# Optimization experiments

Hardware: AMD Instinct MI355X
Metric: run time of the kernel (lower is better)

Reference implementation:

```python
import jax, jax.numpy as jnp
import numpy as np

B, L, C = 16, 450, 768
MID = 256
K = 8912
TEMP = 0.07
ENT_TEMP = 0.01
EPS_NORM = 1e-12


def _l2norm(v):
    n = jnp.sqrt(jnp.sum(v * v, axis=-1, keepdims=True))
    return v / jnp.maximum(n, EPS_NORM)


def setup_inputs() -> dict:
    key = jax.random.key(0)
    k1, k2, k3, k4 = jax.random.split(key, 4)
    x = jax.random.normal(k1, (B, L, C), dtype=jnp.float32)
    W_down = jax.random.normal(k2, (C, MID), dtype=jnp.float32) * (1.0 / np.sqrt(C))
    b_down = jnp.zeros((MID,), dtype=jnp.float32)
    bound = 1.0 / np.sqrt(MID)
    embedding = jax.random.uniform(k3, (K, MID), dtype=jnp.float32, minval=-bound, maxval=bound)
    return {"x": x, "W_down": W_down, "b_down": b_down, "embedding": embedding}


def reference(x, W_down, b_down, embedding):
    Bx, Lx, Cx = x.shape
    # down projection: [B,L,C] -> [B,L,MID]
    z = jnp.einsum('blc,cm->blm', x, W_down) + b_down
    zf = z.reshape(Bx * Lx, MID)
    zn = _l2norm(zf)                       # [N, MID]
    en = _l2norm(embedding)                # [K, MID]
    # squared euclidean distance on the unit sphere: ||a-b||^2 = 2 - 2 a.b
    d = 2.0 - 2.0 * jnp.einsum('nm,km->nk', zn, en)   # [N, K]
    idx = jnp.argmin(d, axis=1)            # [N]
    # codebook usage (no-grad stats)
    occ = jnp.bincount(idx, length=K)
    code_book_usage = jnp.mean((occ > 0).astype(jnp.float32))
    # soft assignment probs (hard_quant branch)
    logits = -d / TEMP
    probs = jax.nn.softmax(logits, axis=1)
    z_q = en[idx]                          # [N, MID]
    vq_loss = jnp.mean((z_q - jax.lax.stop_gradient(zn)) ** 2)
    commit_loss = jnp.mean((jax.lax.stop_gradient(z_q) - zn) ** 2)
    # straight-through estimator
    z_q_ste = zn + jax.lax.stop_gradient(z_q - zn)
    # entropy loss on affinity = -d at entropy temperature
    fa = -d / ENT_TEMP
    p = jax.nn.softmax(fa, axis=-1)
    lp = jax.nn.log_softmax(fa, axis=-1)
    avg_probs = jnp.mean(p, axis=0)
    avg_entropy = -jnp.sum(avg_probs * jnp.log(avg_probs + 1e-5))
    sample_entropy = -jnp.mean(jnp.sum(p * lp, axis=-1))
    entropy_loss = sample_entropy - avg_entropy
    return (z_q_ste.reshape(Bx, Lx, MID), probs.reshape(Bx, Lx, K),
            code_book_usage, vq_loss, commit_loss, entropy_loss)
```

## Files before the change

### kernel.cpp

```cpp
#include <hip/hip_runtime.h>
#include <stdint.h>

#define N_TOK 7200
#define N_PAD 7232
#define N_PAD_A 7296
#define K_CODE 8912
#define K_PAD 8960
#define N_KT 140
#define NKT128 70
#define NMT128 57
#define MID 256
#define C_DIM 768
#define INV_TEMP (1.0f/0.07f)
#define INV_ETEMP 100.0f
#define MARGIN 0.02f
#define CAND_CAP 64
#define EPS_N 1e-12f

typedef __attribute__((ext_vector_type(8))) short short8;
typedef __attribute__((ext_vector_type(4))) float f32x4;

__device__ __forceinline__ unsigned short f2bf(float f) {
    unsigned u = __float_as_uint(f);
    u += 0x7fffu + ((u >> 16) & 1u);
    return (unsigned short)(u >> 16);
}
__device__ __forceinline__ float bf2f(unsigned short h) {
    return __uint_as_float(((unsigned)h) << 16);
}

__device__ __forceinline__ void gload16(const void* g, void* l) {
    __builtin_amdgcn_global_load_lds(
        (const __attribute__((address_space(1))) unsigned int*)g,
        (__attribute__((address_space(3))) unsigned int*)l,
        16, 0, 0);
}

__global__ void k_prep(const float* __restrict__ emb,
                       float* __restrict__ en, unsigned short* __restrict__ en_h,
                       const float* __restrict__ W,
                       unsigned short* __restrict__ wt_h, unsigned short* __restrict__ wt_l,
                       float* __restrict__ ap_acc, int* __restrict__ used,
                       float* __restrict__ acc4, int* __restrict__ ccnt,
                       unsigned short* __restrict__ zn_h) {
    __shared__ float sb[256];
    int b = blockIdx.x, t = threadIdx.x;
    if (b < K_CODE) {
        float v = emb[b * MID + t];
        sb[t] = v * v; __syncthreads();
        for (int s = 128; s > 0; s >>= 1) { if (t < s) sb[t] += sb[t + s]; __syncthreads(); }
        float nn = sqrtf(sb[0]);
        float o = v / fmaxf(nn, EPS_N);
        en[b * MID + t] = o;
        en_h[b * MID + t] = f2bf(o);
    } else if (b < K_CODE + 768) {
        int i = (b - K_CODE) * 256 + t;
        int c = i / MID, tc = i % MID;
        float v = W[i];
        unsigned short h = f2bf(v);
        unsigned short l = f2bf(v - bf2f(h));
        wt_h[tc * C_DIM + c] = h;
        wt_l[tc * C_DIM + c] = l;
    } else {
        int i = (b - K_CODE - 768) * 256 + t;
        if (i < K_CODE) { ap_acc[i] = 0.f; used[i] = 0; }
        if (i < N_TOK) ccnt[i] = 0;
        if (i < 4) acc4[i] = 0.f;
        for (int j = i; j < (N_PAD_A - N_TOK) * MID; j += 8960) zn_h[(size_t)N_TOK * MID + j] = 0;
        for (int j = i; j < (K_PAD - K_CODE) * MID; j += 8960) en_h[(size_t)K_CODE * MID + j] = 0;
    }
}

__global__ __launch_bounds__(256) void k_zgemm(const float* __restrict__ x,
                                               const unsigned short* __restrict__ wt_h,
                                               const unsigned short* __restrict__ wt_l,
                                               float* __restrict__ zbuf) {
    __shared__ unsigned short ls[4 * 64 * 72];
    unsigned short* xh = ls;
    unsigned short* xl = ls + 64 * 72;
    unsigned short* wh = ls + 2 * 64 * 72;
    unsigned short* wl = ls + 3 * 64 * 72;
    int tid = threadIdx.x;
    int m0 = blockIdx.y * 64;
    int t0 = blockIdx.x * 64;
    int lane = tid & 63, wv = tid >> 6;
    int quad = lane >> 4, l15 = lane & 15;
    int mrow0 = (wv >> 1) * 32, ncol0 = (wv & 1) * 32;
    f32x4 acc[2][2] = {};

    for (int ch = 0; ch < 12; ch++) {
        int c0 = ch * 64;
        for (int it = 0; it < 4; it++) {
            int r = it * 16 + (tid >> 4);
            int cq = tid & 15;
            float4 v = make_float4(0.f, 0.f, 0.f, 0.f);
            int gr = m0 + r;
            if (gr < N_TOK) v = ((const float4*)x)[(size_t)gr * (C_DIM / 4) + (c0 >> 2) + cq];
            unsigned short h0 = f2bf(v.x), h1 = f2bf(v.y), h2 = f2bf(v.z), h3 = f2bf(v.w);
            ushort4 hh = make_ushort4(h0, h1, h2, h3);
            ushort4 ll = make_ushort4(f2bf(v.x - bf2f(h0)), f2bf(v.y - bf2f(h1)),
                                      f2bf(v.z - bf2f(h2)), f2bf(v.w - bf2f(h3)));
            *((ushort4*)&xh[r * 72 + cq * 4]) = hh;
            *((ushort4*)&xl[r * 72 + cq * 4]) = ll;
        }
        for (int it = 0; it < 2; it++) {
            int r = it * 32 + (tid >> 3);
            int cq = tid & 7;
            uint4 vh = ((const uint4*)wt_h)[(size_t)(t0 + r) * (C_DIM / 8) + (c0 >> 3) + cq];
            uint4 vl = ((const uint4*)wt_l)[(size_t)(t0 + r) * (C_DIM / 8) + (c0 >> 3) + cq];
            *((uint4*)&wh[r * 72 + cq * 8]) = vh;
            *((uint4*)&wl[r * 72 + cq * 8]) = vl;
        }
        __syncthreads();
        for (int ks = 0; ks < 2; ks++) {
            int co = ks * 32 + quad * 8;
            short8 ah0 = *((const short8*)&xh[(mrow0 + l15) * 72 + co]);
            short8 ah1 = *((const short8*)&xh[(mrow0 + 16 + l15) * 72 + co]);
            short8 al0 = *((const short8*)&xl[(mrow0 + l15) * 72 + co]);
            short8 al1 = *((const short8*)&xl[(mrow0 + 16 + l15) * 72 + co]);
            short8 bh0 = *((const short8*)&wh[(ncol0 + l15) * 72 + co]);
            short8 bh1 = *((const short8*)&wh[(ncol0 + 16 + l15) * 72 + co]);
            short8 bl0 = *((const short8*)&wl[(ncol0 + l15) * 72 + co]);
            short8 bl1 = *((const short8*)&wl[(ncol0 + 16 + l15) * 72 + co]);
            acc[0][0] = __builtin_amdgcn_mfma_f32_16x16x32_bf16(ah0, bh0, acc[0][0], 0, 0, 0);
            acc[0][1] = __builtin_amdgcn_mfma_f32_16x16x32_bf16(ah0, bh1, acc[0][1], 0, 0, 0);
            acc[1][0] = __builtin_amdgcn_mfma_f32_16x16x32_bf16(ah1, bh0, acc[1][0], 0, 0, 0);
            acc[1][1] = __builtin_amdgcn_mfma_f32_16x16x32_bf16(ah1, bh1, acc[1][1], 0, 0, 0);
            acc[0][0] = __builtin_amdgcn_mfma_f32_16x16x32_bf16(ah0, bl0, acc[0][0], 0, 0, 0);
            acc[0][1] = __builtin_amdgcn_mfma_f32_16x16x32_bf16(ah0, bl1, acc[0][1], 0, 0, 0);
            acc[1][0] = __builtin_amdgcn_mfma_f32_16x16x32_bf16(ah1, bl0, acc[1][0], 0, 0, 0);
            acc[1][1] = __builtin_amdgcn_mfma_f32_16x16x32_bf16(ah1, bl1, acc[1][1], 0, 0, 0);
            acc[0][0] = __builtin_amdgcn_mfma_f32_16x16x32_bf16(al0, bh0, acc[0][0], 0, 0, 0);
            acc[0][1] = __builtin_amdgcn_mfma_f32_16x16x32_bf16(al0, bh1, acc[0][1], 0, 0, 0);
            acc[1][0] = __builtin_amdgcn_mfma_f32_16x16x32_bf16(al1, bh0, acc[1][0], 0, 0, 0);
            acc[1][1] = __builtin_amdgcn_mfma_f32_16x16x32_bf16(al1, bh1, acc[1][1], 0, 0, 0);
        }
        __syncthreads();
    }
    for (int i = 0; i < 2; i++)
        for (int j = 0; j < 2; j++)
            for (int r = 0; r < 4; r++) {
                int gr = m0 + mrow0 + i * 16 + quad * 4 + r;
                int gc = t0 + ncol0 + j * 16 + l15;
                if (gr < N_TOK) zbuf[(size_t)gr * MID + gc] = acc[i][j][r];
            }
}

__global__ void k_znorm(float* __restrict__ zbuf, const float* __restrict__ b_down,
                        unsigned short* __restrict__ zn_h) {
    int n = blockIdx.x, t = threadIdx.x;
    float v = zbuf[(size_t)n * MID + t] + b_down[t];
    __shared__ float sb[256];
    sb[t] = v * v; __syncthreads();
    for (int s = 128; s > 0; s >>= 1) { if (t < s) sb[t] += sb[t + s]; __syncthreads(); }
    float nn = sqrtf(sb[0]);
    float o = v / fmaxf(nn, EPS_N);
    zbuf[(size_t)n * MID + t] = o;
    zn_h[(size_t)n * MID + t] = f2bf(o);
}

template<int PASS>
__global__ __launch_bounds__(256) void k_dpass(const unsigned short* __restrict__ zn_h,
                                               const unsigned short* __restrict__ en_h,
                                               float4* __restrict__ part4,
                                               const float* __restrict__ rs_m,
                                               const float* __restrict__ rs_ist,
                                               const float* __restrict__ rs_is1,
                                               float* __restrict__ ap_acc,
                                               float* __restrict__ out1,
                                               int* __restrict__ ccnt,
                                               int* __restrict__ cand) {
    __shared__ __align__(16) char lds[2 * 32768];
    int tid = threadIdx.x;
    {
    }
    int flat = blockIdx.x * NMT128 + blockIdx.y;
    const int NW = NKT128 * NMT128;
    const int q = NW >> 3, r8 = NW & 7;
    int xcd = flat & 7, sidx = flat >> 3;
    int wg = (xcd < r8 ? xcd * (q + 1) : r8 * (q + 1) + (xcd - r8) * q) + sidx;
    int kt = wg / NMT128, mt = wg - kt * NMT128;
    int m0 = mt * 128, k0 = kt * 128;
    int lane = tid & 63, wv = tid >> 6;
    int quad = lane >> 4, l15 = lane & 15;
    int wr = wv >> 1, wc = wv & 1;
    f32x4 acc[4][4] = {};

    int sr = tid >> 3;
    int scb = (tid & 7) * 16;

    auto stage = [&](int step, int buf) {
        int cB = step * 128;
        char* base = lds + buf * 32768;
        #pragma unroll
        for (int it = 0; it < 4; it++) {
            int r = it * 32 + sr;
            int srcb = scb ^ ((r & 7) << 4);
            gload16((const char*)zn_h + (size_t)(m0 + r) * 512 + cB + srcb,
                    base + it * 4096 + wv * 1024);
            gload16((const char*)en_h + (size_t)(k0 + r) * 512 + cB + srcb,
                    base + 16384 + it * 4096 + wv * 1024);
        }
    };

    stage(0, 0);
    __syncthreads();
    int cur = 0;
    for (int step = 0; step < 4; step++) {
        if (step < 3) stage(step + 1, cur ^ 1);
        const char* lA = lds + cur * 32768;
        const char* lB = lA + 16384;
        #pragma unroll
        for (int ks = 0; ks < 2; ks++) {
            short8 a[4], b[4];
            #pragma unroll
            for (int i = 0; i < 4; i++) {
                int ra = wr * 64 + i * 16 + l15;
                int ca = (ks * 64 + quad * 16) ^ ((ra & 7) << 4);
                a[i] = *(const short8*)(lA + ra * 128 + ca);
                int rb = wc * 64 + i * 16 + l15;
                int cb2 = (ks * 64 + quad * 16) ^ ((rb & 7) << 4);
                b[i] = *(const short8*)(lB + rb * 128 + cb2);
            }
            #pragma unroll
            for (int i = 0; i < 4; i++)
                #pragma unroll
                for (int j = 0; j < 4; j++)
                    acc[i][j] = __builtin_amdgcn_mfma_f32_16x16x32_bf16(a[i], b[j], acc[i][j], 0, 0, 0);
        }
        __syncthreads();
        cur ^= 1;
    }

    if (PASS == 1) {
        int kth = kt * 2 + wc;
        #pragma unroll
        for (int i = 0; i < 4; i++) {
            #pragma unroll
            for (int r = 0; r < 4; r++) {
                float dv[4]; float vmin = 1e30f;
                #pragma unroll
                for (int j = 0; j < 4; j++) {
                    int gc = k0 + wc * 64 + j * 16 + l15;
                    float d = 2.f - 2.f * acc[i][j][r];
                    dv[j] = (gc < K_CODE) ? d : 1e30f;
                    vmin = fminf(vmin, dv[j]);
                }
                vmin = fminf(vmin, __shfl_xor(vmin, 1));
                vmin = fminf(vmin, __shfl_xor(vmin, 2));
                vmin = fminf(vmin, __shfl_xor(vmin, 4));
                vmin = fminf(vmin, __shfl_xor(vmin, 8));
                float st = 0.f, s1 = 0.f, s2 = 0.f;
                #pragma unroll
                for (int j = 0; j < 4; j++) {
                    float dd = vmin - dv[j];
                    st += __expf(dd * INV_TEMP);
                    float te = dd * INV_ETEMP;
                    float e = __expf(te);
                    s1 += e; s2 += e * te;
                }
                st += __shfl_xor(st, 1); st += __shfl_xor(st, 2);
                st += __shfl_xor(st, 4); st += __shfl_xor(st, 8);
                s1 += __shfl_xor(s1, 1); s1 += __shfl_xor(s1, 2);
                s1 += __shfl_xor(s1, 4); s1 += __shfl_xor(s1, 8);
                s2 += __shfl_xor(s2, 1); s2 += __shfl_xor(s2, 2);
                s2 += __shfl_xor(s2, 4); s2 += __shfl_xor(s2, 8);
                if (l15 == 0) {
                    int gr = m0 + wr * 64 + i * 16 + quad * 4 + r;
                    if (gr < N_TOK) part4[(size_t)gr * N_KT + kth] = make_float4(vmin, st, s1, s2);
                }
            }
        }
    } else {
        float* lm = (float*)lds;
        float* lt_ = lm + 128;
        float* l1_ = lt_ + 128;
        float* colacc = l1_ + 128;
        if (tid < 128) {
            int gr = m0 + tid;
            bool ok = gr < N_TOK;
            lm[tid]  = ok ? rs_m[gr]   : 0.f;
            lt_[tid] = ok ? rs_ist[gr] : 0.f;
            l1_[tid] = ok ? rs_is1[gr] : 0.f;
        }
        __syncthreads();
        float ce[4] = {0.f, 0.f, 0.f, 0.f};
        #pragma unroll
        for (int i = 0; i < 4; i++) {
            #pragma unroll
            for (int r = 0; r < 4; r++) {
                int lr = wr * 64 + i * 16 + quad * 4 + r;
                int gr = m0 + lr;
                float m_ = lm[lr], t_ = lt_[lr], i1 = l1_[lr];
                bool okr = gr < N_TOK;
                float thr = m_ + MARGIN;
                #pragma unroll
                for (int j = 0; j < 4; j++) {
                    int gc = k0 + wc * 64 + j * 16 + l15;
                    if (okr && gc < K_CODE) {
                        float d = 2.f - 2.f * acc[i][j][r];
                        ce[j] += __expf((m_ - d) * INV_ETEMP) * i1;
                        float p = __expf((m_ - d) * INV_TEMP) * t_;
                        out1[(size_t)gr * K_CODE + gc] = p;
                        if (d <= thr) {
                            int pd = atomicAdd(&ccnt[gr], 1);
                            if (pd < CAND_CAP) cand[gr * CAND_CAP + pd] = gc;
                        }
                    }
                }
            }
        }
        #pragma unroll
        for (int j = 0; j < 4; j++) {
            ce[j] += __shfl_xor(ce[j], 16);
            ce[j] += __shfl_xor(ce[j], 32);
        }
        if (quad == 0) {
            #pragma unroll
            for (int j = 0; j < 4; j++)
                colacc[wr * 128 + wc * 64 + j * 16 + l15] = ce[j];
        }
        __syncthreads();
        if (tid < 128) {
            int gc = k0 + tid;
            if (gc < K_CODE) atomicAdd(&ap_acc[gc], colacc[tid] + colacc[128 + tid]);
        }
    }
}

__global__ void k_combine(const float4* __restrict__ part4,
                          float* __restrict__ rs_m, float* __restrict__ rs_ist,
                          float* __restrict__ rs_is1,
                          float* __restrict__ acc4) {
    int sub = threadIdx.x >> 6;
    int row = blockIdx.x * 4 + sub;
    int l = threadIdx.x & 63;
    float4 pv[3];
    float m = 1e30f;
    #pragma unroll
    for (int c = 0; c < 3; c++) {
        int t = l + c * 64;
        pv[c] = (t < N_KT) ? part4[(size_t)row * N_KT + t] : make_float4(1e30f, 0.f, 0.f, 0.f);
        m = fminf(m, pv[c].x);
    }
    #pragma unroll
    for (int s = 1; s < 64; s <<= 1) m = fminf(m, __shfl_xor(m, s));
    float st = 0.f, s1 = 0.f, s2 = 0.f;
    #pragma unroll
    for (int c = 0; c < 3; c++) {
        float mb = pv[c].x;
        int t = l + c * 64;
        if (t < N_KT && mb < 1e29f) {
            float dT = (m - mb) * INV_TEMP;
            st += __expf(dT) * pv[c].y;
            float dE = (m - mb) * INV_ETEMP;
            float e = __expf(dE);
            s1 += e * pv[c].z;
            s2 += e * (pv[c].w + dE * pv[c].z);
        }
    }
    #pragma unroll
    for (int s = 1; s < 64; s <<= 1) {
        st += __shfl_xor(st, s);
        s1 += __shfl_xor(s1, s);
        s2 += __shfl_xor(s2, s);
    }
    if (l == 0) {
        rs_m[row] = m;
        rs_ist[row] = 1.f / st;
        rs_is1[row] = 1.f / s1;
        atomicAdd(&acc4[1], s2 / s1 - __logf(s1));
    }
}

__global__ void k_refine(const float* __restrict__ zn, const float* __restrict__ en,
                         const int* __restrict__ ccnt, const int* __restrict__ cand,
                         int* __restrict__ idxb, int* __restrict__ used,
                         float* __restrict__ acc4, float* __restrict__ out0) {
    int n = blockIdx.x * 4 + (threadIdx.x >> 6);
    int lane = threadIdx.x & 63;
    if (n >= N_TOK) return;
    int cnt = ccnt[n];
    if (cnt > CAND_CAP) cnt = CAND_CAP;
    float4 a = ((const float4*)(zn + (size_t)n * MID))[lane];
    float best = 1e30f; int bj = K_CODE;
    for (int c = 0; c < cnt; c++) {
        int code = cand[n * CAND_CAP + c];
        float4 b = ((const float4*)(en + (size_t)code * MID))[lane];
        float s = a.x * b.x + a.y * b.y + a.z * b.z + a.w * b.w;
        #pragma unroll
        for (int off = 1; off < 64; off <<= 1) s += __shfl_xor(s, off);
        float dist = 2.f - 2.f * s;
        if (dist < best || (dist == best && code < bj)) { best = dist; bj = code; }
    }
    float4 b = ((const float4*)(en + (size_t)bj * MID))[lane];
    ((float4*)(out0 + (size_t)n * MID))[lane] = b;
    float dx = b.x - a.x, dy = b.y - a.y, dz = b.z - a.z, dw = b.w - a.w;
    float sq = dx * dx + dy * dy + dz * dz + dw * dw;
    #pragma unroll
    for (int off = 32; off > 0; off >>= 1) sq += __shfl_down(sq, off);
    if (lane == 0) {
        idxb[n] = bj;
        used[bj] = 1;
        atomicAdd(&acc4[0], sq);
    }
}

__global__ void k_scal(const int* __restrict__ used, const float* __restrict__ ap_acc,
                       const float* __restrict__ acc4, float* __restrict__ outs) {
    int t = threadIdx.x;
    float uSum = 0.f, aeSum = 0.f;
    for (int k = t; k < K_CODE; k += 256) {
        uSum += (float)used[k];
        float ap = ap_acc[k] * (1.0f / (float)N_TOK);
        aeSum += ap * __logf(ap + 1e-5f);
    }
    __shared__ float sb[256];
    sb[t] = uSum; __syncthreads();
    for (int s = 128; s > 0; s >>= 1) { if (t < s) sb[t] += sb[t + s]; __syncthreads(); }
    uSum = sb[0];
    __syncthreads(); sb[t] = aeSum; __syncthreads();
    for (int s = 128; s > 0; s >>= 1) { if (t < s) sb[t] += sb[t + s]; __syncthreads(); }
    aeSum = sb[0];
    if (t == 0) {
        outs[0] = uSum / (float)K_CODE;
        float vq = acc4[0] / (float)((size_t)N_TOK * MID);
        outs[1] = vq;
        outs[2] = vq;
        outs[3] = -(acc4[1] / (float)N_TOK) + aeSum;
    }
}

extern "C" void kernel_launch(void* const* d_in, const int* in_sizes, int n_in,
                              void* d_out, int out_size, void* d_ws, size_t ws_size,
                              hipStream_t stream) {
    const float* x   = (const float*)d_in[0];
    const float* W   = (const float*)d_in[1];
    const float* b   = (const float*)d_in[2];
    const float* emb = (const float*)d_in[3];

    float* out  = (float*)d_out;
    float* out0 = out;
    float* out1 = out + (size_t)N_TOK * MID;
    float* outs = out + (size_t)N_TOK * MID + (size_t)N_TOK * K_CODE;

    char* w = (char*)d_ws;
    size_t off = 0;
    auto carve = [&](size_t bytes) { void* p = w + off; off += (bytes + 255) & ~(size_t)255; return p; };
    float*          zn    = (float*)         carve((size_t)N_PAD * MID * 4);
    float*          en    = (float*)         carve((size_t)K_PAD * MID * 4);
    unsigned short* zn_h  = (unsigned short*)carve((size_t)N_PAD_A * MID * 2);
    unsigned short* en_h  = (unsigned short*)carve((size_t)K_PAD * MID * 2);
    unsigned short* wt_h  = (unsigned short*)carve((size_t)MID * C_DIM * 2);
    unsigned short* wt_l  = (unsigned short*)carve((size_t)MID * C_DIM * 2);
    float4*         part4 = (float4*)        carve((size_t)N_TOK * N_KT * 16);
    float*          rs_m  = (float*)         carve((size_t)N_TOK * 4);
    float*          rs_ist= (float*)         carve((size_t)N_TOK * 4);
    float*          rs_is1= (float*)         carve((size_t)N_TOK * 4);
    int*            ccnt  = (int*)           carve((size_t)N_TOK * 4);
    int*            cand  = (int*)           carve((size_t)N_TOK * CAND_CAP * 4);
    int*            idxb  = (int*)           carve((size_t)N_TOK * 4);
    float*          ap_acc= (float*)         carve((size_t)K_CODE * 4);
    int*            used  = (int*)           carve((size_t)K_CODE * 4);
    float*          acc4  = (float*)         carve(16);
    (void)ws_size; (void)in_sizes; (void)n_in; (void)out_size;

    k_prep   <<<K_CODE + 768 + 35, 256, 0, stream>>>(emb, en, en_h, W, wt_h, wt_l,
                                                     ap_acc, used, acc4, ccnt, zn_h);
    k_zgemm  <<<dim3(4, 113), 256, 0, stream>>>(x, wt_h, wt_l, zn);
    k_znorm  <<<N_TOK, 256, 0, stream>>>(zn, b, zn_h);
    k_dpass<1><<<dim3(NKT128, NMT128), 256, 0, stream>>>(zn_h, en_h, part4, rs_m, rs_ist, rs_is1, ap_acc, out1, ccnt, cand);
    k_combine<<<N_TOK / 4, 256, 0, stream>>>(part4, rs_m, rs_ist, rs_is1, acc4);
    k_dpass<2><<<dim3(NKT128, NMT128), 256, 0, stream>>>(zn_h, en_h, part4, rs_m, rs_ist, rs_is1, ap_acc, out1, ccnt, cand);
    k_refine <<<N_TOK / 4, 256, 0, stream>>>(zn, en, ccnt, cand, idxb, used, acc4, out0);
    k_scal   <<<1, 256, 0, stream>>>(used, ap_acc, acc4, outs);
}
```

Measured before the change: 708.5 us.

## Store distances once and replace second GEMM pass with elementwise finalize kernel

Instead of recomputing the N×K distance GEMM in a second pass, the first GEMM now writes raw distances into the probs output buffer. A new streaming kernel then reads them back and writes softmax probs in place, along with column entropy sums and candidate lists. The GEMM also drops LDS double buffering in favour of a single buffer with plain synchronisation. This trades a full GEMM recompute for an extra read/write of the ~256MB output, and the GEMM loses load/compute overlap.

```diff
diff --git a/kernel.cpp b/kernel.cpp
--- a/kernel.cpp
+++ b/kernel.cpp
@@ -159,21 +159,12 @@
     zn_h[(size_t)n * MID + t] = f2bf(o);
 }
 
-template<int PASS>
-__global__ __launch_bounds__(256) void k_dpass(const unsigned short* __restrict__ zn_h,
+__global__ __launch_bounds__(256) void k_dgemm(const unsigned short* __restrict__ zn_h,
                                                const unsigned short* __restrict__ en_h,
                                                float4* __restrict__ part4,
-                                               const float* __restrict__ rs_m,
-                                               const float* __restrict__ rs_ist,
-                                               const float* __restrict__ rs_is1,
-                                               float* __restrict__ ap_acc,
-                                               float* __restrict__ out1,
-                                               int* __restrict__ ccnt,
-                                               int* __restrict__ cand) {
-    __shared__ __align__(16) char lds[2 * 32768];
+                                               float* __restrict__ out1) {
+    __shared__ __align__(16) char lds[32768];
     int tid = threadIdx.x;
-    {
-    }
     int flat = blockIdx.x * NMT128 + blockIdx.y;
     const int NW = NKT128 * NMT128;
     const int q = NW >> 3, r8 = NW & 7;
@@ -189,27 +180,18 @@
     int sr = tid >> 3;
     int scb = (tid & 7) * 16;
 
-    auto stage = [&](int step, int buf) {
+    for (int step = 0; step < 4; step++) {
         int cB = step * 128;
-        char* base = lds + buf * 32768;
         #pragma unroll
         for (int it = 0; it < 4; it++) {
             int r = it * 32 + sr;
             int srcb = scb ^ ((r & 7) << 4);
             gload16((const char*)zn_h + (size_t)(m0 + r) * 512 + cB + srcb,
-                    base + it * 4096 + wv * 1024);
+                    lds + it * 4096 + wv * 1024);
             gload16((const char*)en_h + (size_t)(k0 + r) * 512 + cB + srcb,
-                    base + 16384 + it * 4096 + wv * 1024);
-        }
-    };
-
-    stage(0, 0);
-    __syncthreads();
-    int cur = 0;
-    for (int step = 0; step < 4; step++) {
-        if (step < 3) stage(step + 1, cur ^ 1);
-        const char* lA = lds + cur * 32768;
-        const char* lB = lA + 16384;
+                    lds + 16384 + it * 4096 + wv * 1024);
+        }
+        __syncthreads();
         #pragma unroll
         for (int ks = 0; ks < 2; ks++) {
             short8 a[4], b[4];
@@ -217,10 +199,10 @@
             for (int i = 0; i < 4; i++) {
                 int ra = wr * 64 + i * 16 + l15;
                 int ca = (ks * 64 + quad * 16) ^ ((ra & 7) << 4);
-                a[i] = *(const short8*)(lA + ra * 128 + ca);
+                a[i] = *(const short8*)(lds + ra * 128 + ca);
                 int rb = wc * 64 + i * 16 + l15;
                 int cb2 = (ks * 64 + quad * 16) ^ ((rb & 7) << 4);
-                b[i] = *(const short8*)(lB + rb * 128 + cb2);
+                b[i] = *(const short8*)(lds + 16384 + rb * 128 + cb2);
             }
             #pragma unroll
             for (int i = 0; i < 4; i++)
@@ -229,101 +211,47 @@
                     acc[i][j] = __builtin_amdgcn_mfma_f32_16x16x32_bf16(a[i], b[j], acc[i][j], 0, 0, 0);
         }
         __syncthreads();
-        cur ^= 1;
-    }
-
-    if (PASS == 1) {
-        int kth = kt * 2 + wc;
+    }
+
+    int kth = kt * 2 + wc;
+    #pragma unroll
+    for (int i = 0; i < 4; i++) {
         #pragma unroll
-        for (int i = 0; i < 4; i++) {
+        for (int r = 0; r < 4; r++) {
+            int gr = m0 + wr * 64 + i * 16 + quad * 4 + r;
+            bool okr = gr < N_TOK;
+            float dv[4]; float vmin = 1e30f;
             #pragma unroll
-            for (int r = 0; r < 4; r++) {
-                float dv[4]; float vmin = 1e30f;
-                #pragma unroll
-                for (int j = 0; j < 4; j++) {
-                    int gc = k0 + wc * 64 + j * 16 + l15;
-                    float d = 2.f - 2.f * acc[i][j][r];
-                    dv[j] = (gc < K_CODE) ? d : 1e30f;
-                    vmin = fminf(vmin, dv[j]);
-                }
-                vmin = fminf(vmin, __shfl_xor(vmin, 1));
-                vmin = fminf(vmin, __shfl_xor(vmin, 2));
-                vmin = fminf(vmin, __shfl_xor(vmin, 4));
-                vmin = fminf(vmin, __shfl_xor(vmin, 8));
-                float st = 0.f, s1 = 0.f, s2 = 0.f;
-                #pragma unroll
-                for (int j = 0; j < 4; j++) {
-                    float dd = vmin - dv[j];
-                    st += __expf(dd * INV_TEMP);
-                    float te = dd * INV_ETEMP;
-                    float e = __expf(te);
-                    s1 += e; s2 += e * te;
-                }
-                st += __shfl_xor(st, 1); st += __shfl_xor(st, 2);
-                st += __shfl_xor(st, 4); st += __shfl_xor(st, 8);
-                s1 += __shfl_xor(s1, 1); s1 += __shfl_xor(s1, 2);
-                s1 += __shfl_xor(s1, 4); s1 += __shfl_xor(s1, 8);
-                s2 += __shfl_xor(s2, 1); s2 += __shfl_xor(s2, 2);
-                s2 += __shfl_xor(s2, 4); s2 += __shfl_xor(s2, 8);
-                if (l15 == 0) {
-                    int gr = m0 + wr * 64 + i * 16 + quad * 4 + r;
-                    if (gr < N_TOK) part4[(size_t)gr * N_KT + kth] = make_float4(vmin, st, s1, s2);
-                }
+            for (int j = 0; j < 4; j++) {
+                int gc = k0 + wc * 64 + j * 16 + l15;
+                float d = 2.f - 2.f * acc[i][j][r];
+                bool okc = gc < K_CODE;
+                dv[j] = okc ? d : 1e30f;
+                vmin = fminf(vmin, dv[j]);
+                if (okr && okc) out1[(size_t)gr * K_CODE + gc] = d;
             }
-        }
-    } else {
-        float* lm = (float*)lds;
-        float* lt_ = lm + 128;
-        float* l1_ = lt_ + 128;
-        float* colacc = l1_ + 128;
-        if (tid < 128) {
-            int gr = m0 + tid;
-            bool ok = gr < N_TOK;
-            lm[tid]  = ok ? rs_m[gr]   : 0.f;
-            lt_[tid] = ok ? rs_ist[gr] : 0.f;
-            l1_[tid] = ok ? rs_is1[gr] : 0.f;
-        }
-        __syncthreads();
-        float ce[4] = {0.f, 0.f, 0.f, 0.f};
-        #pragma unroll
-        for (int i = 0; i < 4; i++) {
+            vmin = fminf(vmin, __shfl_xor(vmin, 1));
+            vmin = fminf(vmin, __shfl_xor(vmin, 2));
+            vmin = fminf(vmin, __shfl_xor(vmin, 4));
+            vmin = fminf(vmin, __shfl_xor(vmin, 8));
+            float st = 0.f, s1 = 0.f, s2 = 0.f;
             #pragma unroll
-            for (int r = 0; r < 4; r++) {
-                int lr = wr * 64 + i * 16 + quad * 4 + r;
-                int gr = m0 + lr;
-                float m_ = lm[lr], t_ = lt_[lr], i1 = l1_[lr];
-                bool okr = gr < N_TOK;
-                float thr = m_ + MARGIN;
-                #pragma unroll
-                for (int j = 0; j < 4; j++) {
-                    int gc = k0 + wc * 64 + j * 16 + l15;
-                    if (okr && gc < K_CODE) {
-                        float d = 2.f - 2.f * acc[i][j][r];
-                        ce[j] += __expf((m_ - d) * INV_ETEMP) * i1;
-                        float p = __expf((m_ - d) * INV_TEMP) * t_;
-                        out1[(size_t)gr * K_CODE + gc] = p;
-                        if (d <= thr) {
-                            int pd = atomicAdd(&ccnt[gr], 1);
-                            if (pd < CAND_CAP) cand[gr * CAND_CAP + pd] = gc;
-                        }
-                    }
-                }
+            for (int j = 0; j < 4; j++) {
+                float dd = vmin - dv[j];
+                st += __expf(dd * INV_TEMP);
+                float te = dd * INV_ETEMP;
+                float e = __expf(te);
+                s1 += e; s2 += e * te;
             }
-        }
-        #pragma unroll
-        for (int j = 0; j < 4; j++) {
-            ce[j] += __shfl_xor(ce[j], 16);
-            ce[j] += __shfl_xor(ce[j], 32);
-        }
-        if (quad == 0) {
-            #pragma unroll
-            for (int j = 0; j < 4; j++)
-                colacc[wr * 128 + wc * 64 + j * 16 + l15] = ce[j];
-        }
-        __syncthreads();
-        if (tid < 128) {
-            int gc = k0 + tid;
-            if (gc < K_CODE) atomicAdd(&ap_acc[gc], colacc[tid] + colacc[128 + tid]);
+            st += __shfl_xor(st, 1); st += __shfl_xor(st, 2);
+            st += __shfl_xor(st, 4); st += __shfl_xor(st, 8);
+            s1 += __shfl_xor(s1, 1); s1 += __shfl_xor(s1, 2);
+            s1 += __shfl_xor(s1, 4); s1 += __shfl_xor(s1, 8);
+            s2 += __shfl_xor(s2, 1); s2 += __shfl_xor(s2, 2);
+            s2 += __shfl_xor(s2, 4); s2 += __shfl_xor(s2, 8);
+            if (l15 == 0 && okr) {
+                part4[(size_t)gr * N_KT + kth] = make_float4(vmin, st, s1, s2);
+            }
         }
     }
 }
@@ -370,6 +298,67 @@
         rs_ist[row] = 1.f / st;
         rs_is1[row] = 1.f / s1;
         atomicAdd(&acc4[1], s2 / s1 - __logf(s1));
+    }
+}
+
+__global__ __launch_bounds__(256) void k_final(float* __restrict__ out1,
+                                               const float* __restrict__ rs_m,
+                                               const float* __restrict__ rs_ist,
+                                               const float* __restrict__ rs_is1,
+                                               float* __restrict__ ap_acc,
+                                               int* __restrict__ ccnt,
+                                               int* __restrict__ cand) {
+    __shared__ float lm[128], lt_[128], l1_[128];
+    __shared__ float colacc[4 * 256];
+    int ct = blockIdx.x, rt = blockIdx.y;
+    int r0 = rt * 128, c0 = ct * 256;
+    int t = threadIdx.x;
+    if (t < 128) {
+        int gr = r0 + t;
+        bool ok = gr < N_TOK;
+        lm[t]  = ok ? rs_m[gr]   : 0.f;
+        lt_[t] = ok ? rs_ist[gr] : 0.f;
+        l1_[t] = ok ? rs_is1[gr] : 0.f;
+    }
+    __syncthreads();
+    int g = t >> 6;
+    int cq = (t & 63) * 4;
+    int gc = c0 + cq;
+    float ce0 = 0.f, ce1 = 0.f, ce2 = 0.f, ce3 = 0.f;
+    if (gc < K_CODE) {
+        for (int i = 0; i < 32; i++) {
+            int lr = g * 32 + i;
+            int gr = r0 + lr;
+            if (gr >= N_TOK) break;
+            size_t base = (size_t)gr * K_CODE + gc;
+            float4 d = *(const float4*)(out1 + base);
+            float m_ = lm[lr], tt = lt_[lr], i1 = l1_[lr];
+            float thr = m_ + MARGIN;
+            ce0 += __expf((m_ - d.x) * INV_ETEMP) * i1;
+            ce1 += __expf((m_ - d.y) * INV_ETEMP) * i1;
+            ce2 += __expf((m_ - d.z) * INV_ETEMP) * i1;
+            ce3 += __expf((m_ - d.w) * INV_ETEMP) * i1;
+            float4 p;
+            p.x = __expf((m_ - d.x) * INV_TEMP) * tt;
+            p.y = __expf((m_ - d.y) * INV_TEMP) * tt;
+            p.z = __expf((m_ - d.z) * INV_TEMP) * tt;
+            p.w = __expf((m_ - d.w) * INV_TEMP) * tt;
+            *((float4*)(out1 + base)) = p;
+            if (d.x <= thr) { int pd = atomicAdd(&ccnt[gr], 1); if (pd < CAND_CAP) cand[gr * CAND_CAP + pd] = gc + 0; }
+            if (d.y <= thr) { int pd = atomicAdd(&ccnt[gr], 1); if (pd < CAND_CAP) cand[gr * CAND_CAP + pd] = gc + 1; }
+            if (d.z <= thr) { int pd = atomicAdd(&ccnt[gr], 1); if (pd < CAND_CAP) cand[gr * CAND_CAP + pd] = gc + 2; }
+            if (d.w <= thr) { int pd = atomicAdd(&ccnt[gr], 1); if (pd < CAND_CAP) cand[gr * CAND_CAP + pd] = gc + 3; }
+        }
+    }
+    colacc[g * 256 + cq + 0] = ce0;
+    colacc[g * 256 + cq + 1] = ce1;
+    colacc[g * 256 + cq + 2] = ce2;
+    colacc[g * 256 + cq + 3] = ce3;
+    __syncthreads();
+    {
+        float s = colacc[t] + colacc[256 + t] + colacc[512 + t] + colacc[768 + t];
+        int c = c0 + t;
+        if (c < K_CODE) atomicAdd(&ap_acc[c], s);
     }
 }
 
@@ -469,9 +458,9 @@
                                                      ap_acc, used, acc4, ccnt, zn_h);
     k_zgemm  <<<dim3(4, 113), 256, 0, stream>>>(x, wt_h, wt_l, zn);
     k_znorm  <<<N_TOK, 256, 0, stream>>>(zn, b, zn_h);
-    k_dpass<1><<<dim3(NKT128, NMT128), 256, 0, stream>>>(zn_h, en_h, part4, rs_m, rs_ist, rs_is1, ap_acc, out1, ccnt, cand);
+    k_dgemm  <<<dim3(NKT128, NMT128), 256, 0, stream>>>(zn_h, en_h, part4, out1);
     k_combine<<<N_TOK / 4, 256, 0, stream>>>(part4, rs_m, rs_ist, rs_is1, acc4);
-    k_dpass<2><<<dim3(NKT128, NMT128), 256, 0, stream>>>(zn_h, en_h, part4, rs_m, rs_ist, rs_is1, ap_acc, out1, ccnt, cand);
+    k_final  <<<dim3(35, 57), 256, 0, stream>>>(out1, rs_m, rs_ist, rs_is1, ap_acc, ccnt, cand);
     k_refine <<<N_TOK / 4, 256, 0, stream>>>(zn, en, ccnt, cand, idxb, used, acc4, out0);
     k_scal   <<<1, 256, 0, stream>>>(used, ap_acc, acc4, outs);
 }
```

New measurement: 717.2 us. No clear change (+1.2%).
